# Performance work log

Measured on AMD Instinct MI355X. Metric: run time of the kernel, lower is better.

## Reference

```python
import jax, jax.numpy as jnp
import numpy as np

PAD_IDX, BOS_IDX, EOS_IDX = 0, 1, 2
NUM_LABELS = 48
B, T = 1024, 512
NEG = -10000.0


def make_trans(key):
    trans = jax.random.normal(key, (NUM_LABELS, NUM_LABELS), dtype=jnp.float32)
    trans = trans.at[BOS_IDX, :].set(NEG)
    trans = trans.at[:, EOS_IDX].set(NEG)
    trans = trans.at[:, PAD_IDX].set(NEG)
    trans = trans.at[PAD_IDX, :].set(NEG)
    trans = trans.at[PAD_IDX, EOS_IDX].set(0.0)
    trans = trans.at[PAD_IDX, PAD_IDX].set(0.0)
    return trans


def setup_inputs() -> dict:
    key = jax.random.key(0)
    k_h, k_tr = jax.random.split(key)
    h = jax.random.normal(k_h, (B, T, NUM_LABELS), dtype=jnp.float32)
    mask = jnp.ones((B, T), dtype=jnp.float32)
    trans = make_trans(k_tr)
    return {"h": h, "mask": mask, "trans": trans, "batch_size": B}


def reference(h, mask, trans, batch_size):
    # h: (B, T, L), mask: (B, T), trans: (L, L)
    L = trans.shape[0]
    score0 = jnp.full((batch_size, L), NEG, dtype=h.dtype).at[:, BOS_IDX].set(0.0)

    def step(score, inp):
        h_t, m_t = inp            # h_t: (B, L), m_t: (B,)
        # new[b, i] = logsumexp_j(score[b, j] + h_t[b, i] + trans[i, j])
        z = score[:, None, :] + h_t[:, :, None] + trans[None, :, :]  # (B, L, L)
        score_t = jax.nn.logsumexp(z, axis=-1)
        m = m_t[:, None]
        score = score_t * m + score * (1.0 - m)
        return score, None

    # scan over time: move T to leading axis
    score, _ = jax.lax.scan(step, score0, (jnp.swapaxes(h, 0, 1), jnp.swapaxes(mask, 0, 1)))
    return jax.nn.logsumexp(score, axis=-1)  # (B,)
```

## Files before the change

### kernel.cpp

```cpp
#include <hip/hip_runtime.h>
#include <math.h>

namespace {
constexpr int L = 48;
constexpr int OCT = 8;
constexpr float LN2f = 0.69314718055994530942f;
}

template<bool BWD>
__device__ __forceinline__ float half_pass(
    const float* __restrict__ hb, const float* __restrict__ mb,
    const float* __restrict__ trans, int T, int S, int lane,
    int& Mi_out, float& rs_out) {
  const bool active = lane < L;
  const int safelane = active ? lane : 0;

  float E[L];
  if (active) {
#pragma unroll
    for (int j = 0; j < L; ++j)
      E[j] = __expf(trans[BWD ? (j * L + lane) : (lane * L + j)]);
  } else {
#pragma unroll
    for (int j = 0; j < L; ++j) E[j] = 0.0f;
  }

  float p = BWD ? (active ? 1.0f : 0.0f)
                : ((lane == 1) ? 1.0f : 0.0f);
  int Mi = 0;
  float rs = 1.0f;

  const int NOCT = S / OCT;

  float hf[OCT], mf[OCT];
#pragma unroll
  for (int k = 0; k < OCT; ++k) {
    const int t = BWD ? (T - 1 - k) : k;
    hf[k] = hb[t * L + safelane];
    mf[k] = mb[t];
  }

  for (int oct = 0; oct < NOCT; ++oct) {
    float hn[OCT], mn[OCT];
    if (oct + 1 < NOCT) {
#pragma unroll
      for (int k = 0; k < OCT; ++k) {
        const int s = (oct + 1) * OCT + k;
        const int t = BWD ? (T - 1 - s) : s;
        hn[k] = hb[t * L + safelane];
        mn[k] = mb[t];
      }
    } else {
#pragma unroll
      for (int k = 0; k < OCT; ++k) { hn[k] = 0.f; mn[k] = 1.f; }
    }

#pragma unroll
    for (int tt = 0; tt < OCT; ++tt) {
      const bool RENORM = ((tt & 3) == 3);
      const float g = __expf(hf[tt]) * rs;
      const float pr = p * rs;
      rs = 1.0f;

      const float bv = BWD ? (p * g) : p;
      const int pb = __float_as_int(bv);
      float a0 = 0.f, a1 = 0.f, a2 = 0.f, a3 = 0.f;
      unsigned mx = 0u;
#pragma unroll
      for (int j = 0; j < L; j += 4) {
        const int r0 = __builtin_amdgcn_readlane(pb, j + 0);
        const int r1 = __builtin_amdgcn_readlane(pb, j + 1);
        const int r2 = __builtin_amdgcn_readlane(pb, j + 2);
        const int r3 = __builtin_amdgcn_readlane(pb, j + 3);
        a0 = fmaf(__int_as_float(r0), E[j + 0], a0);
        a1 = fmaf(__int_as_float(r1), E[j + 1], a1);
        a2 = fmaf(__int_as_float(r2), E[j + 2], a2);
        a3 = fmaf(__int_as_float(r3), E[j + 3], a3);
        if (RENORM) {
          const unsigned u0 = (unsigned)r0, u1 = (unsigned)r1;
          const unsigned u2 = (unsigned)r2, u3 = (unsigned)r3;
          const unsigned m01 = u0 > u1 ? u0 : u1;
          const unsigned m23 = u2 > u3 ? u2 : u3;
          const unsigned m03 = m01 > m23 ? m01 : m23;
          mx = mx > m03 ? mx : m03;
        }
      }
      const float s = (a0 + a1) + (a2 + a3);
      const float pn = BWD ? s : s * g;
      p = (mf[tt] > 0.5f) ? pn : pr;

      if (RENORM) {
        const int ke = (int)(mx >> 23);
        const bool ok = (ke > 0) && (ke < 255);
        rs = ok ? __uint_as_float((unsigned)(254 - ke) << 23) : 1.0f;
        Mi += ok ? (ke - 127) : 0;
      }
    }
#pragma unroll
    for (int k = 0; k < OCT; ++k) { hf[k] = hn[k]; mf[k] = mn[k]; }
  }
  Mi_out = Mi;
  rs_out = rs;
  return p;
}

__global__ __launch_bounds__(128, 2)
void crf_fwd(const float* __restrict__ h,
             const float* __restrict__ mask,
             const float* __restrict__ trans,
             float* __restrict__ out, int T) {
  const int b = blockIdx.x;
  const int wid = threadIdx.x >> 6;
  const int lane = threadIdx.x & 63;
  const int S = T >> 1;

  const float* __restrict__ hb = h + (size_t)b * T * L;
  const float* __restrict__ mb = mask + (size_t)b * T;

  __shared__ float xq[64];
  __shared__ int xmi;

  int Mi; float rs; float st;
  if (wid == 0) st = half_pass<false>(hb, mb, trans, T, S, lane, Mi, rs);
  else          st = half_pass<true >(hb, mb, trans, T, S, lane, Mi, rs);

  if (wid == 1) {
    xq[lane] = st * rs;
    if (lane == 0) xmi = Mi;
  }
  __syncthreads();
  if (wid == 0) {
    float d = (st * rs) * xq[lane];
#pragma unroll
    for (int off = 32; off; off >>= 1) d += __shfl_xor(d, off, 64);
    if (lane == 0)
      out[b] = ((float)(Mi + xmi) + __log2f(d)) * LN2f;
  }
}

extern "C" void kernel_launch(void* const* d_in, const int* in_sizes, int n_in,
                              void* d_out, int out_size, void* d_ws, size_t ws_size,
                              hipStream_t stream) {
  const float* h     = (const float*)d_in[0];
  const float* mask  = (const float*)d_in[1];
  const float* trans = (const float*)d_in[2];
  float* out = (float*)d_out;
  const int B = out_size;
  const int T = in_sizes[1] / B;
  crf_fwd<<<B, 128, 0, stream>>>(h, mask, trans, out, T);
}
```

Measured before the change: 222.7 us.

## Split each CRF pass across two waves with LDS exchange and packed FMA

Each scan direction (forward/backward half) now runs on two wavefronts instead of one. Two lanes share one output label, each covering half of the j-sum, and the state vector is exchanged through a double-buffered LDS array with a block barrier every step, replacing 48 readlanes per step. Packed float2 FMAs are used, and the renormalisation max is taken from the LDS-loaded vectors. This shortens the serial per-step chain and raises per-block parallelism, at the cost of a __syncthreads per timestep across four waves and a cross-lane shuffle.

```diff
diff --git a/kernel.cpp b/kernel.cpp
--- a/kernel.cpp
+++ b/kernel.cpp
@@ -1,5 +1,8 @@
 #include <hip/hip_runtime.h>
 #include <math.h>
+
+typedef float f32x2 __attribute__((ext_vector_type(2)));
+typedef float f32x4 __attribute__((ext_vector_type(4)));
 
 namespace {
 constexpr int L = 48;
@@ -8,37 +11,46 @@
 }
 
 template<bool BWD>
-__device__ __forceinline__ float half_pass(
+__device__ __forceinline__ float pass_run(
     const float* __restrict__ hb, const float* __restrict__ mb,
-    const float* __restrict__ trans, int T, int S, int lane,
-    int& Mi_out, float& rs_out) {
-  const bool active = lane < L;
-  const int safelane = active ? lane : 0;
+    const float* __restrict__ trans, int T, int S, int l, int ww,
+    float (*pbuf)[64], int& Mi_out, float& rs_out) {
+  const bool act = l < L;
+  const int half = l & 1;
+  const int ip = act ? (ww * 24 + (l >> 1)) : 0;
+  const int wi = act ? (ww * 24 + (l >> 1)) : l;
 
-  float E[L];
-  if (active) {
+  f32x2 Ep[12];
+  if (act) {
 #pragma unroll
-    for (int j = 0; j < L; ++j)
-      E[j] = __expf(trans[BWD ? (j * L + lane) : (lane * L + j)]);
+    for (int k = 0; k < 12; ++k) {
+      const int j0 = half * 24 + 2 * k;
+      const float e0 = __expf(trans[BWD ? ((j0 + 0) * L + ip) : (ip * L + j0 + 0)]);
+      const float e1 = __expf(trans[BWD ? ((j0 + 1) * L + ip) : (ip * L + j0 + 1)]);
+      Ep[k] = (f32x2){e0, e1};
+    }
   } else {
 #pragma unroll
-    for (int j = 0; j < L; ++j) E[j] = 0.0f;
+    for (int k = 0; k < 12; ++k) Ep[k] = (f32x2){0.f, 0.f};
   }
 
-  float p = BWD ? (active ? 1.0f : 0.0f)
-                : ((lane == 1) ? 1.0f : 0.0f);
+  float p = BWD ? (act ? 1.0f : 0.0f)
+                : ((act && ip == 1) ? 1.0f : 0.0f);
   int Mi = 0;
   float rs = 1.0f;
 
   const int NOCT = S / OCT;
-
   float hf[OCT], mf[OCT];
 #pragma unroll
   for (int k = 0; k < OCT; ++k) {
     const int t = BWD ? (T - 1 - k) : k;
-    hf[k] = hb[t * L + safelane];
+    hf[k] = hb[t * L + ip];
     mf[k] = mb[t];
   }
+
+  pbuf[0][wi] = BWD ? p * __expf(hf[0]) : p;
+  __syncthreads();
+  int cur = 0;
 
   for (int oct = 0; oct < NOCT; ++oct) {
     float hn[OCT], mn[OCT];
@@ -47,7 +59,7 @@
       for (int k = 0; k < OCT; ++k) {
         const int s = (oct + 1) * OCT + k;
         const int t = BWD ? (T - 1 - s) : s;
-        hn[k] = hb[t * L + safelane];
+        hn[k] = hb[t * L + ip];
         mn[k] = mb[t];
       }
     } else {
@@ -58,43 +70,54 @@
 #pragma unroll
     for (int tt = 0; tt < OCT; ++tt) {
       const bool RENORM = ((tt & 3) == 3);
-      const float g = __expf(hf[tt]) * rs;
+      const float* src = pbuf[cur];
+      const f32x4 v0 = *(const f32x4*)(src + half * 24 + 0);
+      const f32x4 v1 = *(const f32x4*)(src + half * 24 + 4);
+      const f32x4 v2 = *(const f32x4*)(src + half * 24 + 8);
+      const f32x4 v3 = *(const f32x4*)(src + half * 24 + 12);
+      const f32x4 v4 = *(const f32x4*)(src + half * 24 + 16);
+      const f32x4 v5 = *(const f32x4*)(src + half * 24 + 20);
+
+      f32x2 a0 = v0.xy * Ep[0], a1 = v0.zw * Ep[1];
+      a0 += v1.xy * Ep[2];  a1 += v1.zw * Ep[3];
+      a0 += v2.xy * Ep[4];  a1 += v2.zw * Ep[5];
+      a0 += v3.xy * Ep[6];  a1 += v3.zw * Ep[7];
+      a0 += v4.xy * Ep[8];  a1 += v4.zw * Ep[9];
+      a0 += v5.xy * Ep[10]; a1 += v5.zw * Ep[11];
+      const f32x2 s2 = a0 + a1;
+      const float sh = s2.x + s2.y;
+      const float s = sh + __shfl_xor(sh, 1, 64);
+
+      const float pn = BWD ? s : s * (__expf(hf[tt]) * rs);
       const float pr = p * rs;
+      p = (mf[tt] > 0.5f) ? pn : pr;
       rs = 1.0f;
 
-      const float bv = BWD ? (p * g) : p;
-      const int pb = __float_as_int(bv);
-      float a0 = 0.f, a1 = 0.f, a2 = 0.f, a3 = 0.f;
-      unsigned mx = 0u;
-#pragma unroll
-      for (int j = 0; j < L; j += 4) {
-        const int r0 = __builtin_amdgcn_readlane(pb, j + 0);
-        const int r1 = __builtin_amdgcn_readlane(pb, j + 1);
-        const int r2 = __builtin_amdgcn_readlane(pb, j + 2);
-        const int r3 = __builtin_amdgcn_readlane(pb, j + 3);
-        a0 = fmaf(__int_as_float(r0), E[j + 0], a0);
-        a1 = fmaf(__int_as_float(r1), E[j + 1], a1);
-        a2 = fmaf(__int_as_float(r2), E[j + 2], a2);
-        a3 = fmaf(__int_as_float(r3), E[j + 3], a3);
-        if (RENORM) {
-          const unsigned u0 = (unsigned)r0, u1 = (unsigned)r1;
-          const unsigned u2 = (unsigned)r2, u3 = (unsigned)r3;
-          const unsigned m01 = u0 > u1 ? u0 : u1;
-          const unsigned m23 = u2 > u3 ? u2 : u3;
-          const unsigned m03 = m01 > m23 ? m01 : m23;
-          mx = mx > m03 ? mx : m03;
-        }
-      }
-      const float s = (a0 + a1) + (a2 + a3);
-      const float pn = BWD ? s : s * g;
-      p = (mf[tt] > 0.5f) ? pn : pr;
-
       if (RENORM) {
-        const int ke = (int)(mx >> 23);
+        f32x2 m0 = v0.xy, m1 = v0.zw;
+        m0 = (f32x2){fmaxf(m0.x, v1.x), fmaxf(m0.y, v1.y)};
+        m1 = (f32x2){fmaxf(m1.x, v1.z), fmaxf(m1.y, v1.w)};
+        m0 = (f32x2){fmaxf(m0.x, v2.x), fmaxf(m0.y, v2.y)};
+        m1 = (f32x2){fmaxf(m1.x, v2.z), fmaxf(m1.y, v2.w)};
+        m0 = (f32x2){fmaxf(m0.x, v3.x), fmaxf(m0.y, v3.y)};
+        m1 = (f32x2){fmaxf(m1.x, v3.z), fmaxf(m1.y, v3.w)};
+        m0 = (f32x2){fmaxf(m0.x, v4.x), fmaxf(m0.y, v4.y)};
+        m1 = (f32x2){fmaxf(m1.x, v4.z), fmaxf(m1.y, v4.w)};
+        m0 = (f32x2){fmaxf(m0.x, v5.x), fmaxf(m0.y, v5.y)};
+        m1 = (f32x2){fmaxf(m1.x, v5.z), fmaxf(m1.y, v5.w)};
+        float mx = fmaxf(fmaxf(m0.x, m0.y), fmaxf(m1.x, m1.y));
+        mx = fmaxf(mx, __shfl_xor(mx, 1, 64));
+        const unsigned ub = __float_as_uint(mx);
+        const int ke = (int)(ub >> 23);
         const bool ok = (ke > 0) && (ke < 255);
         rs = ok ? __uint_as_float((unsigned)(254 - ke) << 23) : 1.0f;
         Mi += ok ? (ke - 127) : 0;
       }
+
+      const float hnx = (tt < OCT - 1) ? hf[tt + 1] : hn[0];
+      pbuf[cur ^ 1][wi] = BWD ? p * (__expf(hnx) * rs) : p;
+      __syncthreads();
+      cur ^= 1;
     }
 #pragma unroll
     for (int k = 0; k < OCT; ++k) { hf[k] = hn[k]; mf[k] = mn[k]; }
@@ -104,37 +127,42 @@
   return p;
 }
 
-__global__ __launch_bounds__(128, 2)
+__global__ __launch_bounds__(256, 4)
 void crf_fwd(const float* __restrict__ h,
              const float* __restrict__ mask,
              const float* __restrict__ trans,
              float* __restrict__ out, int T) {
   const int b = blockIdx.x;
-  const int wid = threadIdx.x >> 6;
-  const int lane = threadIdx.x & 63;
+  const int wv = threadIdx.x >> 6;
+  const int l = threadIdx.x & 63;
+  const int pass = wv >> 1;
+  const int ww = wv & 1;
   const int S = T >> 1;
+
+  __shared__ __align__(16) float pbuf[2][2][64];
+  __shared__ float fin[2][64];
+  __shared__ int mi_sh[2];
 
   const float* __restrict__ hb = h + (size_t)b * T * L;
   const float* __restrict__ mb = mask + (size_t)b * T;
 
-  __shared__ float xq[64];
-  __shared__ int xmi;
+  int Mi; float rs; float pf;
+  if (pass == 0)
+    pf = pass_run<false>(hb, mb, trans, T, S, l, ww, pbuf[0], Mi, rs);
+  else
+    pf = pass_run<true >(hb, mb, trans, T, S, l, ww, pbuf[1], Mi, rs);
 
-  int Mi; float rs; float st;
-  if (wid == 0) st = half_pass<false>(hb, mb, trans, T, S, lane, Mi, rs);
-  else          st = half_pass<true >(hb, mb, trans, T, S, lane, Mi, rs);
+  const int ip = (l < L) ? (ww * 24 + (l >> 1)) : 0;
+  if (l < L && (l & 1) == 0) fin[pass][ip] = pf * rs;
+  if (ww == 0 && l == 0) mi_sh[pass] = Mi;
+  __syncthreads();
 
-  if (wid == 1) {
-    xq[lane] = st * rs;
-    if (lane == 0) xmi = Mi;
-  }
-  __syncthreads();
-  if (wid == 0) {
-    float d = (st * rs) * xq[lane];
+  if (wv == 0) {
+    float d = (l < L) ? fin[0][l] * fin[1][l] : 0.0f;
 #pragma unroll
     for (int off = 32; off; off >>= 1) d += __shfl_xor(d, off, 64);
-    if (lane == 0)
-      out[b] = ((float)(Mi + xmi) + __log2f(d)) * LN2f;
+    if (l == 0)
+      out[b] = ((float)(mi_sh[0] + mi_sh[1]) + __log2f(d)) * LN2f;
   }
 }
 
@@ -147,5 +175,5 @@
   float* out = (float*)d_out;
   const int B = out_size;
   const int T = in_sizes[1] / B;
-  crf_fwd<<<B, 128, 0, stream>>>(h, mask, trans, out, T);
+  crf_fwd<<<B, 256, 0, stream>>>(h, mask, trans, out, T);
 }
```

Measured after the change: 222.5 us. Within noise of the previous version (-0.1%).

## Exchange CRF state through LDS ping-pong buffers instead of per-lane readlane broadcasts

Applied to the files above, without the earlier changes.

Each lane now writes its current probability to a per-wave double-buffered LDS array. Each step reads the whole 48-entry state vector back with float4 broadcast loads, instead of issuing 48 scalar readlanes per step. The exponentiated transition matrix moves from 48 VGPRs per lane into LDS, stored row per lane with a padded stride of 52, and is read as float4 alongside the state. Accumulation uses packed two-wide float math. The intent is to cut the serialized SALU readlane chain and register pressure. The cost is an LDS store-then-load round trip on every step of the sequential recurrence, which relies on in-wave ordering of LDS accesses without any barrier.

```diff
diff --git a/kernel.cpp b/kernel.cpp
--- a/kernel.cpp
+++ b/kernel.cpp
@@ -1,45 +1,41 @@
 #include <hip/hip_runtime.h>
 #include <math.h>
 
+typedef float f32x2 __attribute__((ext_vector_type(2)));
+typedef float f32x4 __attribute__((ext_vector_type(4)));
+
 namespace {
 constexpr int L = 48;
+constexpr int EST = 52;
 constexpr int OCT = 8;
 constexpr float LN2f = 0.69314718055994530942f;
 }
 
 template<bool BWD>
-__device__ __forceinline__ float half_pass(
+__device__ __forceinline__ float stream_run(
     const float* __restrict__ hb, const float* __restrict__ mb,
-    const float* __restrict__ trans, int T, int S, int lane,
+    const float* __restrict__ Erow, float* __restrict__ pb0,
+    float* __restrict__ pb1, int T, int S, int l,
     int& Mi_out, float& rs_out) {
-  const bool active = lane < L;
-  const int safelane = active ? lane : 0;
+  const bool act = l < L;
+  const int sl = act ? l : 0;
 
-  float E[L];
-  if (active) {
-#pragma unroll
-    for (int j = 0; j < L; ++j)
-      E[j] = __expf(trans[BWD ? (j * L + lane) : (lane * L + j)]);
-  } else {
-#pragma unroll
-    for (int j = 0; j < L; ++j) E[j] = 0.0f;
-  }
-
-  float p = BWD ? (active ? 1.0f : 0.0f)
-                : ((lane == 1) ? 1.0f : 0.0f);
+  float p = BWD ? (act ? 1.0f : 0.0f)
+                : ((l == 1) ? 1.0f : 0.0f);
   int Mi = 0;
   float rs = 1.0f;
-
-  const int NOCT = S / OCT;
 
   float hf[OCT], mf[OCT];
 #pragma unroll
   for (int k = 0; k < OCT; ++k) {
     const int t = BWD ? (T - 1 - k) : k;
-    hf[k] = hb[t * L + safelane];
+    hf[k] = hb[t * L + sl];
     mf[k] = mb[t];
   }
 
+  if (act) pb0[l] = BWD ? p * __expf(hf[0]) : p;
+
+  const int NOCT = S / OCT;
   for (int oct = 0; oct < NOCT; ++oct) {
     float hn[OCT], mn[OCT];
     if (oct + 1 < NOCT) {
@@ -47,7 +43,7 @@
       for (int k = 0; k < OCT; ++k) {
         const int s = (oct + 1) * OCT + k;
         const int t = BWD ? (T - 1 - s) : s;
-        hn[k] = hb[t * L + safelane];
+        hn[k] = hb[t * L + sl];
         mn[k] = mb[t];
       }
     } else {
@@ -57,43 +53,51 @@
 
 #pragma unroll
     for (int tt = 0; tt < OCT; ++tt) {
-      const bool RENORM = ((tt & 3) == 3);
-      const float g = __expf(hf[tt]) * rs;
+      const bool RN = ((tt & 3) == 3);
+      const float* src = (tt & 1) ? pb1 : pb0;
+      float* dst = (tt & 1) ? pb0 : pb1;
+      const f32x4* s4 = (const f32x4*)src;
+      const f32x4* e4 = (const f32x4*)Erow;
+
+      f32x2 a0 = {0.f, 0.f}, a1 = {0.f, 0.f};
+      f32x2 a2 = {0.f, 0.f}, a3 = {0.f, 0.f};
+      f32x4 mx = {0.f, 0.f, 0.f, 0.f};
+#pragma unroll
+      for (int c = 0; c < 12; ++c) {
+        const f32x4 pv = s4[c];
+        const f32x4 ev = e4[c];
+        if (c & 1) { a2 += pv.xy * ev.xy; a3 += pv.zw * ev.zw; }
+        else       { a0 += pv.xy * ev.xy; a1 += pv.zw * ev.zw; }
+        if (RN)
+          mx = (f32x4){fmaxf(mx.x, pv.x), fmaxf(mx.y, pv.y),
+                       fmaxf(mx.z, pv.z), fmaxf(mx.w, pv.w)};
+      }
+      const f32x2 sc = (a0 + a2) + (a1 + a3);
+      const float s = sc.x + sc.y;
+
+      const float g = __expf(hf[tt]);
+      const float pn = BWD ? s : s * (g * rs);
       const float pr = p * rs;
+      p = (mf[tt] > 0.5f) ? pn : pr;
       rs = 1.0f;
 
-      const float bv = BWD ? (p * g) : p;
-      const int pb = __float_as_int(bv);
-      float a0 = 0.f, a1 = 0.f, a2 = 0.f, a3 = 0.f;
-      unsigned mx = 0u;
-#pragma unroll
-      for (int j = 0; j < L; j += 4) {
-        const int r0 = __builtin_amdgcn_readlane(pb, j + 0);
-        const int r1 = __builtin_amdgcn_readlane(pb, j + 1);
-        const int r2 = __builtin_amdgcn_readlane(pb, j + 2);
-        const int r3 = __builtin_amdgcn_readlane(pb, j + 3);
-        a0 = fmaf(__int_as_float(r0), E[j + 0], a0);
-        a1 = fmaf(__int_as_float(r1), E[j + 1], a1);
-        a2 = fmaf(__int_as_float(r2), E[j + 2], a2);
-        a3 = fmaf(__int_as_float(r3), E[j + 3], a3);
-        if (RENORM) {
-          const unsigned u0 = (unsigned)r0, u1 = (unsigned)r1;
-          const unsigned u2 = (unsigned)r2, u3 = (unsigned)r3;
-          const unsigned m01 = u0 > u1 ? u0 : u1;
-          const unsigned m23 = u2 > u3 ? u2 : u3;
-          const unsigned m03 = m01 > m23 ? m01 : m23;
-          mx = mx > m03 ? mx : m03;
-        }
-      }
-      const float s = (a0 + a1) + (a2 + a3);
-      const float pn = BWD ? s : s * g;
-      p = (mf[tt] > 0.5f) ? pn : pr;
-
-      if (RENORM) {
-        const int ke = (int)(mx >> 23);
+      if (RN) {
+        const float m01 = fmaxf(mx.x, mx.y);
+        const float m23 = fmaxf(mx.z, mx.w);
+        const unsigned ub = __float_as_uint(fmaxf(m01, m23));
+        const int ke = (int)(ub >> 23) & 0xFF;
         const bool ok = (ke > 0) && (ke < 255);
         rs = ok ? __uint_as_float((unsigned)(254 - ke) << 23) : 1.0f;
         Mi += ok ? (ke - 127) : 0;
+      }
+
+      if (act) {
+        if (BWD) {
+          const float hnx = (tt < OCT - 1) ? hf[tt + 1] : hn[0];
+          dst[l] = p * (__expf(hnx) * rs);
+        } else {
+          dst[l] = p;
+        }
       }
     }
 #pragma unroll
@@ -110,31 +114,43 @@
              const float* __restrict__ trans,
              float* __restrict__ out, int T) {
   const int b = blockIdx.x;
-  const int wid = threadIdx.x >> 6;
-  const int lane = threadIdx.x & 63;
+  const int w = threadIdx.x >> 6;
+  const int l = threadIdx.x & 63;
+  const bool act = l < L;
   const int S = T >> 1;
 
-  const float* __restrict__ hb = h + (size_t)b * T * L;
-  const float* __restrict__ mb = mask + (size_t)b * T;
+  __shared__ __align__(16) float Elds[2][L * EST];
+  __shared__ __align__(16) float pbuf[2][2][64];
+  __shared__ float fin[64];
+  __shared__ int mi_sh;
 
-  __shared__ float xq[64];
-  __shared__ int xmi;
+  float* E = Elds[w];
+  if (act) {
+    for (int r = 0; r < L; ++r)
+      E[r * EST + l] = __expf(trans[w ? (l * L + r) : (r * L + l)]);
+  }
 
-  int Mi; float rs; float st;
-  if (wid == 0) st = half_pass<false>(hb, mb, trans, T, S, lane, Mi, rs);
-  else          st = half_pass<true >(hb, mb, trans, T, S, lane, Mi, rs);
+  const float* hb = h + (size_t)b * T * L;
+  const float* mb = mask + (size_t)b * T;
+  const int sl = act ? l : 0;
+  const float* Erow = E + sl * EST;
 
-  if (wid == 1) {
-    xq[lane] = st * rs;
-    if (lane == 0) xmi = Mi;
+  int Mi; float rs; float pf;
+  if (w == 0)
+    pf = stream_run<false>(hb, mb, Erow, pbuf[0][0], pbuf[0][1], T, S, l, Mi, rs);
+  else
+    pf = stream_run<true >(hb, mb, Erow, pbuf[1][0], pbuf[1][1], T, S, l, Mi, rs);
+
+  if (w == 1) {
+    if (act) fin[l] = pf * rs;
+    if (l == 0) mi_sh = Mi;
   }
   __syncthreads();
-  if (wid == 0) {
-    float d = (st * rs) * xq[lane];
+  if (w == 0) {
+    float d = act ? (pf * rs) * fin[l] : 0.0f;
 #pragma unroll
     for (int off = 32; off; off >>= 1) d += __shfl_xor(d, off, 64);
-    if (lane == 0)
-      out[b] = ((float)(Mi + xmi) + __log2f(d)) * LN2f;
+    if (l == 0) out[b] = ((float)(Mi + mi_sh) + __log2f(d)) * LN2f;
   }
 }
 
```

Result: faster. 206.1 us (-7.5%).
